# Performance work log

Hardware: AMD Instinct MI355X
Metric: run time of the kernel (lower is better)

The kernel has to match this reference:

```python
import jax, jax.numpy as jnp
import numpy as np

A = 100000          # num atoms
E = 1600000         # num edges
N_SPECIES = 4       # len(atomic_types)
N_RADIAL = 8        # l=1 radial functions (max_radial hyper)
N_PSEUDO = 4        # Alchemical pseudo species
D = N_RADIAL * N_PSEUDO  # embedding_dim = 32
RC = 5.0            # cutoff radius
WIDTH = 0.5         # shifted-cosine width


def setup_inputs() -> dict:
    key = jax.random.key(0)
    ks = jax.random.split(key, 9)
    return {
        "interatomic_vectors": jax.random.normal(ks[0], (E, 3), dtype=jnp.float32),
        "centers": jax.random.randint(ks[1], (E,), 0, A),
        "neighbors": jax.random.randint(ks[2], (E,), 0, A),
        "species": jax.random.randint(ks[3], (A,), 0, N_SPECIES),
        "structures": jnp.sort(jax.random.randint(ks[4], (A,), 0, 64)),
        "atom_index_in_structure": jax.random.randint(ks[5], (A,), 0, A),
        # learned params
        "W_alch": jax.random.normal(ks[6], (N_SPECIES, N_PSEUDO), dtype=jnp.float32) * 0.1,
        "center_embedding": jax.random.normal(ks[7], (N_SPECIES, D), dtype=jnp.float32),
        "W_contract": jax.random.normal(ks[8], (3, D), dtype=jnp.float32) * (1.0 / np.sqrt(D)),
    }


def _shifted_cosine(d):
    # 1 below rc-width, smooth cosine taper to 0 at rc
    inner = RC - WIDTH
    taper = 0.5 * (jnp.cos(jnp.pi * (d - inner) / WIDTH) + 1.0)
    return jnp.where(d < inner, 1.0, jnp.where(d < RC, taper, 0.0))


def reference(interatomic_vectors, centers, neighbors, species, structures,
              atom_index_in_structure, W_alch, center_embedding, W_contract):
    eps = 1e-12
    d = jnp.sqrt(jnp.sum(interatomic_vectors * interatomic_vectors, axis=1) + eps)  # (E,)
    fc = _shifted_cosine(d)                                                         # (E,)
    # Laplacian-eigenstate-style l=1 radial basis: sin(n*pi*d/rc)/d, n=1..N_RADIAL
    n = jnp.arange(1, N_RADIAL + 1, dtype=jnp.float32)
    R = jnp.sin(n[None, :] * (jnp.pi / RC) * d[:, None]) / d[:, None]               # (E, nR)
    # real l=1 spherical harmonics, m order (-1, 0, 1) -> (y, z, x)/d
    Y = interatomic_vectors[:, jnp.array([1, 2, 0])] / d[:, None]                   # (E, 3)
    # alchemical pseudo-species weights of the neighbor
    alch = W_alch[species[neighbors]]                                               # (E, nQ)
    # per-edge expansion coefficients, scattered onto centers
    edge = (fc[:, None, None, None]
            * Y[:, :, None, None]
            * R[:, None, :, None]
            * alch[:, None, None, :])                                               # (E, 3, nR, nQ)
    spex = jax.ops.segment_sum(edge, centers, num_segments=A)                       # (A, 3, nR, nQ)
    x = spex.reshape(A, 3, D)                                                       # reshape(n,q -> n*q)
    x = x * center_embedding[species][:, None, :]                                   # center encoding
    out = jnp.einsum("amd,od->amo", x, W_contract)                                  # (A, 3, 3)
    return out
```

## Files before the change

kernel.cpp:

```cpp
#include <hip/hip_runtime.h>
#include <hip/hip_fp16.h>


constexpr int NSP  = 4;
constexpr int NRAD = 8;
constexpr int NPS  = 4;
constexpr int DDIM = NRAD * NPS;

constexpr int APB       = 128;
constexpr int APB_SH    = 7;
constexpr int NBIN_PAD  = 832;
constexpr int NROWS_PAD = 832;
constexpr int RS        = 840;
constexpr int PH1_BLK   = 512;
constexpr int PH1_U     = 4;
constexpr int PH1_REC   = PH1_BLK * PH1_U;
constexpr int CAP2      = 1536;
constexpr int IT2       = CAP2 / 256;

__device__ __forceinline__ unsigned pack2(float a, float b) {
    union { __half2 h; unsigned u; } cv;
    cv.h = __floats2half2_rn(a, b);
    return cv.u;
}
__device__ __forceinline__ float2 unpack2(unsigned u) {
    union { unsigned u; __half2 h; } cv;
    cv.u = u;
    return __half22float2(cv.h);
}

__device__ __forceinline__ void build_w2(
    float* sW2, const float* cemb, const float* Wc, const float* W_alch,
    int tid, int nthreads)
{
    for (int i = tid; i < 3 * NRAD * 16; i += nthreads) {
        int p  = i & 15;
        int n  = (i >> 4) & 7;
        int o  = i >> 7;
        int sc = p >> 2, sn = p & 3;
        float w = 0.0f;
        #pragma unroll
        for (int q = 0; q < NPS; q++)
            w += cemb[sc * DDIM + n * NPS + q] * Wc[o * DDIM + n * NPS + q]
               * W_alch[sn * NPS + q];
        sW2[i] = w;
    }
}

__device__ __forceinline__ bool edge_math(
    float vx, float vy, float vz, int pair, const float* sW2,
    float g[3], float t[3])
{
    float d2    = vx * vx + vy * vy + vz * vz + 1e-12f;
    float d     = sqrtf(d2);
    float inv_d = 1.0f / d;

    const float PI = 3.14159265358979323846f;
    const float RCUT = 5.0f, INNER = 4.5f, INVW = 2.0f;
    if (d >= RCUT) return false;
    float taper = 0.5f * (__cosf(PI * (d - INNER) * INVW) + 1.0f);
    float fc = (d < INNER) ? 1.0f : taper;

    float theta = (PI / RCUT) * d;
    float s1 = __sinf(theta);
    float c1 = __cosf(theta);
    float two_c = 2.0f * c1;
    float R[NRAD];
    R[0] = s1 * inv_d;
    float sm2 = 0.0f, sm1 = s1;
    #pragma unroll
    for (int n = 1; n < NRAD; n++) {
        float s = two_c * sm1 - sm2;
        sm2 = sm1; sm1 = s;
        R[n] = s * inv_d;
    }

    #pragma unroll
    for (int o = 0; o < 3; o++) {
        float acc = 0.0f;
        #pragma unroll
        for (int n = 0; n < NRAD; n++)
            acc += R[n] * sW2[(o * NRAD + n) * 16 + pair];
        t[o] = acc;
    }
    g[0] = fc * vy * inv_d;
    g[1] = fc * vz * inv_d;
    g[2] = fc * vx * inv_d;
    return true;
}

__global__ __launch_bounds__(PH1_BLK) void vb_phase1(
    const float* __restrict__ vecs,
    const int*   __restrict__ centers,
    const int*   __restrict__ neighbors,
    const int*   __restrict__ species,
    const float* __restrict__ W_alch,
    const float* __restrict__ cemb,
    const float* __restrict__ Wc,
    unsigned short* __restrict__ runoff,
    int4*        __restrict__ payload,
    int E, int nbin)
{
    __shared__ float sW2[3 * NRAD * 16];
    __shared__ int4  srec[PH1_REC];
    __shared__ unsigned lcntP[NBIN_PAD / 2];
    __shared__ unsigned short lexcl[NBIN_PAD];
    __shared__ int sTotal;

    int tid = threadIdx.x;
    build_w2(sW2, cemb, Wc, W_alch, tid, PH1_BLK);
    for (int i = tid; i < NBIN_PAD / 2; i += PH1_BLK) lcntP[i] = 0;
    __syncthreads();

    int4 rec[PH1_U];
    int  rnk[PH1_U];
    #pragma unroll
    for (int u = 0; u < PH1_U; u++) {
        int e = blockIdx.x * PH1_REC + u * PH1_BLK + tid;
        rec[u].x = -1;
        rnk[u]   = 0;
        if (e < E) {
            float vx = vecs[3 * e + 0];
            float vy = vecs[3 * e + 1];
            float vz = vecs[3 * e + 2];
            int c  = centers[e];
            int pair = species[c] * 4 + species[neighbors[e]];
            float g[3], t[3];
            if (edge_math(vx, vy, vz, pair, sW2, g, t)) {
                rec[u].x = c;
                rec[u].y = (int)pack2(g[0], g[1]);
                rec[u].z = (int)pack2(g[2], t[0]);
                rec[u].w = (int)pack2(t[1], t[2]);
                int bin = c >> APB_SH;
                int sh  = (bin & 1) << 4;
                unsigned old = atomicAdd(&lcntP[bin >> 1], 1u << sh);
                rnk[u] = (int)((old >> sh) & 0xffff);
            }
        }
    }
    __syncthreads();

    if (tid < 64) {
        int base = tid * 13;
        int pre[13];
        int sum = 0;
        #pragma unroll
        for (int j = 0; j < 13; j++) {
            int b = base + j;
            int n = (lcntP[b >> 1] >> ((b & 1) << 4)) & 0xffff;
            pre[j] = sum; sum += n;
        }
        int incl = sum;
        #pragma unroll
        for (int off = 1; off < 64; off <<= 1) {
            int t = __shfl_up(incl, off, 64);
            if (tid >= off) incl += t;
        }
        int ex = incl - sum;
        #pragma unroll
        for (int j = 0; j < 13; j++)
            lexcl[base + j] = (unsigned short)(ex + pre[j]);
        if (tid == 63) sTotal = incl;
    }
    __syncthreads();

    #pragma unroll
    for (int u = 0; u < PH1_U; u++) {
        if (rec[u].x >= 0) {
            int bin = rec[u].x >> APB_SH;
            srec[(int)lexcl[bin] + rnk[u]] = rec[u];
        }
    }
    __syncthreads();

    int total = sTotal;
    size_t pbase = (size_t)blockIdx.x * PH1_REC;
    for (int i = tid; i < total; i += PH1_BLK)
        payload[pbase + i] = srec[i];
    unsigned short* ro = runoff + (size_t)blockIdx.x * RS;
    for (int b = tid; b <= nbin; b += PH1_BLK)
        ro[b] = (b < nbin) ? lexcl[b] : (unsigned short)total;
}

__global__ __launch_bounds__(256) void vb_phase2(
    const unsigned short* __restrict__ runoff,
    const int4*           __restrict__ payload,
    float*                __restrict__ out,
    int A, int nblocks)
{
    __shared__ int4 srec2[CAP2];
    __shared__ unsigned short sidx[CAP2];
    __shared__ unsigned short rid[CAP2];
    __shared__ unsigned short sst[NROWS_PAD];
    __shared__ unsigned short roff[NROWS_PAD + 64];
    __shared__ int cnt[APB], aexcl[APB];
    __shared__ float sout[APB * 9];
    __shared__ int sTotal;

    int b   = blockIdx.x;
    int tid = threadIdx.x;

    for (int r = tid; r < NROWS_PAD; r += 256) {
        unsigned short s0 = 0, len = 0;
        if (r < nblocks) {
            const unsigned short* row = runoff + (size_t)r * RS + b;
            s0  = row[0];
            len = (unsigned short)(row[1] - row[0]);
        }
        sst[r]  = s0;
        roff[r] = len;
    }
    __syncthreads();

    if (tid < 64) {
        int base = tid * 13;
        int pre[13];
        int sum = 0;
        #pragma unroll
        for (int j = 0; j < 13; j++) { pre[j] = sum; sum += roff[base + j]; }
        int incl = sum;
        #pragma unroll
        for (int off = 1; off < 64; off <<= 1) {
            int t = __shfl_up(incl, off, 64);
            if (tid >= off) incl += t;
        }
        int ex = incl - sum;
        #pragma unroll
        for (int j = 0; j < 13; j++)
            roff[base + j] = (unsigned short)(ex + pre[j]);
        if (tid == 63) sTotal = incl;
    }
    __syncthreads();
    if (tid == 0) roff[NROWS_PAD] = (unsigned short)sTotal;
    __syncthreads();

    int total = sTotal;
    float acc[9] = {0,0,0,0,0,0,0,0,0};
    int half = tid >> 7;
    int atom = tid & (APB - 1);

    for (int w0 = 0; w0 < total; w0 += CAP2) {
        int wend = min(w0 + CAP2, total);
        int nc = wend - w0;

        if (tid < APB) cnt[tid] = 0;
        for (int r = tid; r < nblocks; r += 256) {
            int s  = max((int)roff[r], w0);
            int e2 = min((int)roff[r + 1], wend);
            for (int p = s; p < e2; p++)
                rid[p - w0] = (unsigned short)r;
        }
        __syncthreads();

        int key6[IT2], rnk6[IT2];
        #pragma unroll
        for (int it = 0; it < IT2; it++) {
            int i = it * 256 + tid;
            key6[it] = -1;
            rnk6[it] = 0;
            if (i < nc) {
                int p = w0 + i;
                int l = (int)rid[i];
                int j = p - (int)roff[l];
                int4 r = payload[(size_t)l * PH1_REC + (int)sst[l] + j];
                srec2[i] = r;
                int k = r.x & (APB - 1);
                key6[it] = k;
                rnk6[it] = atomicAdd(&cnt[k], 1);
            }
        }
        __syncthreads();

        if (tid < 64) {
            int c0 = cnt[2 * tid], c1 = cnt[2 * tid + 1];
            int s1 = c0 + c1;
            int incl = s1;
            #pragma unroll
            for (int off = 1; off < 64; off <<= 1) {
                int t = __shfl_up(incl, off, 64);
                if (tid >= off) incl += t;
            }
            int ex = incl - s1;
            aexcl[2 * tid]     = ex;
            aexcl[2 * tid + 1] = ex + c0;
        }
        __syncthreads();

        #pragma unroll
        for (int it = 0; it < IT2; it++) {
            if (key6[it] >= 0)
                sidx[aexcl[key6[it]] + rnk6[it]] =
                    (unsigned short)(it * 256 + tid);
        }
        __syncthreads();

        {
            int st = aexcl[atom], n = cnt[atom];
            int mid = st + ((n + 1) >> 1);
            int lo = half ? mid : st;
            int hi = half ? (st + n) : mid;
            for (int j = lo; j < hi; j++) {
                int4 r = srec2[sidx[j]];
                float2 g01 = unpack2((unsigned)r.y);
                float2 g2t = unpack2((unsigned)r.z);
                float2 t12 = unpack2((unsigned)r.w);
                float g0 = g01.x, g1 = g01.y, g2 = g2t.x;
                float t0 = g2t.y, t1 = t12.x, t2 = t12.y;
                acc[0] += g0 * t0; acc[1] += g0 * t1; acc[2] += g0 * t2;
                acc[3] += g1 * t0; acc[4] += g1 * t1; acc[5] += g1 * t2;
                acc[6] += g2 * t0; acc[7] += g2 * t1; acc[8] += g2 * t2;
            }
        }
        __syncthreads();
    }

    if (half == 0) {
        #pragma unroll
        for (int k = 0; k < 9; k++) sout[atom * 9 + k] = acc[k];
    }
    __syncthreads();
    if (half == 1) {
        #pragma unroll
        for (int k = 0; k < 9; k++) sout[atom * 9 + k] += acc[k];
    }
    __syncthreads();
    size_t gbase = (size_t)b * APB * 9;
    size_t lim = (size_t)A * 9;
    for (int i = tid; i < APB * 9; i += 256) {
        size_t gi = gbase + i;
        if (gi < lim) out[gi] = sout[i];
    }
}

__global__ __launch_bounds__(256) void vb_edge_fallback(
    const float* __restrict__ vecs,
    const int*   __restrict__ centers,
    const int*   __restrict__ neighbors,
    const int*   __restrict__ species,
    const float* __restrict__ W_alch,
    const float* __restrict__ cemb,
    const float* __restrict__ Wc,
    float*       __restrict__ out,
    int E)
{
    __shared__ float sW2[3 * NRAD * 16];
    build_w2(sW2, cemb, Wc, W_alch, threadIdx.x, blockDim.x);
    __syncthreads();

    int e = blockIdx.x * blockDim.x + threadIdx.x;
    if (e >= E) return;
    float vx = vecs[3 * e + 0], vy = vecs[3 * e + 1], vz = vecs[3 * e + 2];
    int c = centers[e];
    int pair = species[c] * 4 + species[neighbors[e]];
    float g[3], t[3];
    if (!edge_math(vx, vy, vz, pair, sW2, g, t)) return;
    float* op = out + (size_t)c * 9;
    #pragma unroll
    for (int m = 0; m < 3; m++)
        #pragma unroll
        for (int o = 0; o < 3; o++)
            atomicAdd(op + m * 3 + o, g[m] * t[o]);
}

extern "C" void kernel_launch(void* const* d_in, const int* in_sizes, int n_in,
                              void* d_out, int out_size, void* d_ws, size_t ws_size,
                              hipStream_t stream) {
    const float* vecs      = (const float*)d_in[0];
    const int*   centers   = (const int*)d_in[1];
    const int*   neighbors = (const int*)d_in[2];
    const int*   species   = (const int*)d_in[3];
    const float* W_alch    = (const float*)d_in[6];
    const float* cemb      = (const float*)d_in[7];
    const float* Wc        = (const float*)d_in[8];
    float*       out       = (float*)d_out;

    int E = in_sizes[1];
    int A = in_sizes[3];
    int nbin    = (A + APB - 1) >> APB_SH;
    int nblocks = (E + PH1_REC - 1) / PH1_REC;

    size_t ro_bytes = ((size_t)nblocks * RS * 2 + 255) & ~(size_t)255;
    size_t need = ro_bytes + (size_t)nblocks * PH1_REC * 16;

    if (nbin + 1 <= RS && nbin <= NBIN_PAD && nblocks <= NROWS_PAD &&
        need <= ws_size) {
        unsigned short* runoff = (unsigned short*)d_ws;
        int4* payload = (int4*)((char*)d_ws + ro_bytes);

        vb_phase1<<<nblocks, PH1_BLK, 0, stream>>>(vecs, centers, neighbors,
                                                   species, W_alch, cemb, Wc,
                                                   runoff, payload, E, nbin);
        vb_phase2<<<nbin, 256, 0, stream>>>(runoff, payload, out, A, nblocks);
    } else {
        hipMemsetAsync(d_out, 0, (size_t)out_size * sizeof(float), stream);
        int grid = (E + 255) / 256;
        vb_edge_fallback<<<grid, 256, 0, stream>>>(vecs, centers, neighbors,
                                                   species, W_alch, cemb, Wc,
                                                   out, E);
    }
}
```

Baseline: 129.6 us.

## Bucket records by bin with global atomics and accumulate via shared atomics

```diff
diff --git a/kernel.cpp b/kernel.cpp
--- a/kernel.cpp
+++ b/kernel.cpp
@@ -10,13 +10,10 @@
 constexpr int APB       = 128;
 constexpr int APB_SH    = 7;
 constexpr int NBIN_PAD  = 832;
-constexpr int NROWS_PAD = 832;
-constexpr int RS        = 840;
 constexpr int PH1_BLK   = 512;
 constexpr int PH1_U     = 4;
 constexpr int PH1_REC   = PH1_BLK * PH1_U;
-constexpr int CAP2      = 1536;
-constexpr int IT2       = CAP2 / 256;
+constexpr int BSTR      = 2560;
 
 __device__ __forceinline__ unsigned pack2(float a, float b) {
     union { __half2 h; unsigned u; } cv;
@@ -97,7 +94,7 @@
     const float* __restrict__ W_alch,
     const float* __restrict__ cemb,
     const float* __restrict__ Wc,
-    unsigned short* __restrict__ runoff,
+    unsigned*    __restrict__ gcnt,
     int4*        __restrict__ payload,
     int E, int nbin)
 {
@@ -105,6 +102,7 @@
     __shared__ int4  srec[PH1_REC];
     __shared__ unsigned lcntP[NBIN_PAD / 2];
     __shared__ unsigned short lexcl[NBIN_PAD];
+    __shared__ unsigned short gbase[NBIN_PAD];
     __shared__ int sTotal;
 
     int tid = threadIdx.x;
@@ -171,163 +169,58 @@
             srec[(int)lexcl[bin] + rnk[u]] = rec[u];
         }
     }
+
+    for (int b = tid; b < nbin; b += PH1_BLK) {
+        int n = (int)((lcntP[b >> 1] >> ((b & 1) << 4)) & 0xffff);
+        if (n) gbase[b] = (unsigned short)atomicAdd(&gcnt[b], (unsigned)n);
+    }
     __syncthreads();
 
     int total = sTotal;
-    size_t pbase = (size_t)blockIdx.x * PH1_REC;
-    for (int i = tid; i < total; i += PH1_BLK)
-        payload[pbase + i] = srec[i];
-    unsigned short* ro = runoff + (size_t)blockIdx.x * RS;
-    for (int b = tid; b <= nbin; b += PH1_BLK)
-        ro[b] = (b < nbin) ? lexcl[b] : (unsigned short)total;
+    for (int i = tid; i < total; i += PH1_BLK) {
+        int4 r  = srec[i];
+        int bin = r.x >> APB_SH;
+        int slot = (int)gbase[bin] + (i - (int)lexcl[bin]);
+        if (slot < BSTR)
+            payload[(size_t)bin * BSTR + slot] = r;
+    }
 }
 
 __global__ __launch_bounds__(256) void vb_phase2(
-    const unsigned short* __restrict__ runoff,
-    const int4*           __restrict__ payload,
-    float*                __restrict__ out,
-    int A, int nblocks)
-{
-    __shared__ int4 srec2[CAP2];
-    __shared__ unsigned short sidx[CAP2];
-    __shared__ unsigned short rid[CAP2];
-    __shared__ unsigned short sst[NROWS_PAD];
-    __shared__ unsigned short roff[NROWS_PAD + 64];
-    __shared__ int cnt[APB], aexcl[APB];
+    const unsigned* __restrict__ gcnt,
+    const int4*     __restrict__ payload,
+    float*          __restrict__ out,
+    int A)
+{
     __shared__ float sout[APB * 9];
-    __shared__ int sTotal;
 
     int b   = blockIdx.x;
     int tid = threadIdx.x;
 
-    for (int r = tid; r < NROWS_PAD; r += 256) {
-        unsigned short s0 = 0, len = 0;
-        if (r < nblocks) {
-            const unsigned short* row = runoff + (size_t)r * RS + b;
-            s0  = row[0];
-            len = (unsigned short)(row[1] - row[0]);
-        }
-        sst[r]  = s0;
-        roff[r] = len;
-    }
-    __syncthreads();
-
-    if (tid < 64) {
-        int base = tid * 13;
-        int pre[13];
-        int sum = 0;
-        #pragma unroll
-        for (int j = 0; j < 13; j++) { pre[j] = sum; sum += roff[base + j]; }
-        int incl = sum;
-        #pragma unroll
-        for (int off = 1; off < 64; off <<= 1) {
-            int t = __shfl_up(incl, off, 64);
-            if (tid >= off) incl += t;
-        }
-        int ex = incl - sum;
-        #pragma unroll
-        for (int j = 0; j < 13; j++)
-            roff[base + j] = (unsigned short)(ex + pre[j]);
-        if (tid == 63) sTotal = incl;
-    }
-    __syncthreads();
-    if (tid == 0) roff[NROWS_PAD] = (unsigned short)sTotal;
-    __syncthreads();
-
-    int total = sTotal;
-    float acc[9] = {0,0,0,0,0,0,0,0,0};
-    int half = tid >> 7;
-    int atom = tid & (APB - 1);
-
-    for (int w0 = 0; w0 < total; w0 += CAP2) {
-        int wend = min(w0 + CAP2, total);
-        int nc = wend - w0;
-
-        if (tid < APB) cnt[tid] = 0;
-        for (int r = tid; r < nblocks; r += 256) {
-            int s  = max((int)roff[r], w0);
-            int e2 = min((int)roff[r + 1], wend);
-            for (int p = s; p < e2; p++)
-                rid[p - w0] = (unsigned short)r;
-        }
-        __syncthreads();
-
-        int key6[IT2], rnk6[IT2];
-        #pragma unroll
-        for (int it = 0; it < IT2; it++) {
-            int i = it * 256 + tid;
-            key6[it] = -1;
-            rnk6[it] = 0;
-            if (i < nc) {
-                int p = w0 + i;
-                int l = (int)rid[i];
-                int j = p - (int)roff[l];
-                int4 r = payload[(size_t)l * PH1_REC + (int)sst[l] + j];
-                srec2[i] = r;
-                int k = r.x & (APB - 1);
-                key6[it] = k;
-                rnk6[it] = atomicAdd(&cnt[k], 1);
-            }
-        }
-        __syncthreads();
-
-        if (tid < 64) {
-            int c0 = cnt[2 * tid], c1 = cnt[2 * tid + 1];
-            int s1 = c0 + c1;
-            int incl = s1;
-            #pragma unroll
-            for (int off = 1; off < 64; off <<= 1) {
-                int t = __shfl_up(incl, off, 64);
-                if (tid >= off) incl += t;
-            }
-            int ex = incl - s1;
-            aexcl[2 * tid]     = ex;
-            aexcl[2 * tid + 1] = ex + c0;
-        }
-        __syncthreads();
-
-        #pragma unroll
-        for (int it = 0; it < IT2; it++) {
-            if (key6[it] >= 0)
-                sidx[aexcl[key6[it]] + rnk6[it]] =
-                    (unsigned short)(it * 256 + tid);
-        }
-        __syncthreads();
-
-        {
-            int st = aexcl[atom], n = cnt[atom];
-            int mid = st + ((n + 1) >> 1);
-            int lo = half ? mid : st;
-            int hi = half ? (st + n) : mid;
-            for (int j = lo; j < hi; j++) {
-                int4 r = srec2[sidx[j]];
-                float2 g01 = unpack2((unsigned)r.y);
-                float2 g2t = unpack2((unsigned)r.z);
-                float2 t12 = unpack2((unsigned)r.w);
-                float g0 = g01.x, g1 = g01.y, g2 = g2t.x;
-                float t0 = g2t.y, t1 = t12.x, t2 = t12.y;
-                acc[0] += g0 * t0; acc[1] += g0 * t1; acc[2] += g0 * t2;
-                acc[3] += g1 * t0; acc[4] += g1 * t1; acc[5] += g1 * t2;
-                acc[6] += g2 * t0; acc[7] += g2 * t1; acc[8] += g2 * t2;
-            }
-        }
-        __syncthreads();
-    }
-
-    if (half == 0) {
-        #pragma unroll
-        for (int k = 0; k < 9; k++) sout[atom * 9 + k] = acc[k];
-    }
-    __syncthreads();
-    if (half == 1) {
-        #pragma unroll
-        for (int k = 0; k < 9; k++) sout[atom * 9 + k] += acc[k];
-    }
-    __syncthreads();
-    size_t gbase = (size_t)b * APB * 9;
+    for (int i = tid; i < APB * 9; i += 256) sout[i] = 0.0f;
+    __syncthreads();
+
+    int n = min((int)gcnt[b], BSTR);
+    const int4* seg = payload + (size_t)b * BSTR;
+    for (int i = tid; i < n; i += 256) {
+        int4 r = seg[i];
+        int atom = r.x & (APB - 1);
+        float2 g01 = unpack2((unsigned)r.y);
+        float2 g2t = unpack2((unsigned)r.z);
+        float2 t12 = unpack2((unsigned)r.w);
+        float g0 = g01.x, g1 = g01.y, g2 = g2t.x;
+        float t0 = g2t.y, t1 = t12.x, t2 = t12.y;
+        float* s = &sout[atom * 9];
+        atomicAdd(s + 0, g0 * t0); atomicAdd(s + 1, g0 * t1); atomicAdd(s + 2, g0 * t2);
+        atomicAdd(s + 3, g1 * t0); atomicAdd(s + 4, g1 * t1); atomicAdd(s + 5, g1 * t2);
+        atomicAdd(s + 6, g2 * t0); atomicAdd(s + 7, g2 * t1); atomicAdd(s + 8, g2 * t2);
+    }
+    __syncthreads();
+
+    size_t gbase2 = (size_t)b * APB * 9;
     size_t lim = (size_t)A * 9;
     for (int i = tid; i < APB * 9; i += 256) {
-        size_t gi = gbase + i;
+        size_t gi = gbase2 + i;
         if (gi < lim) out[gi] = sout[i];
     }
 }
@@ -379,18 +272,18 @@
     int nbin    = (A + APB - 1) >> APB_SH;
     int nblocks = (E + PH1_REC - 1) / PH1_REC;
 
-    size_t ro_bytes = ((size_t)nblocks * RS * 2 + 255) & ~(size_t)255;
-    size_t need = ro_bytes + (size_t)nblocks * PH1_REC * 16;
-
-    if (nbin + 1 <= RS && nbin <= NBIN_PAD && nblocks <= NROWS_PAD &&
-        need <= ws_size) {
-        unsigned short* runoff = (unsigned short*)d_ws;
-        int4* payload = (int4*)((char*)d_ws + ro_bytes);
-
+    size_t gc_bytes = ((size_t)nbin * 4 + 255) & ~(size_t)255;
+    size_t need = gc_bytes + (size_t)nbin * BSTR * 16;
+
+    if (nbin <= NBIN_PAD && need <= ws_size) {
+        unsigned* gcnt = (unsigned*)d_ws;
+        int4* payload = (int4*)((char*)d_ws + gc_bytes);
+
+        hipMemsetAsync(gcnt, 0, (size_t)nbin * 4, stream);
         vb_phase1<<<nblocks, PH1_BLK, 0, stream>>>(vecs, centers, neighbors,
                                                    species, W_alch, cemb, Wc,
-                                                   runoff, payload, E, nbin);
-        vb_phase2<<<nbin, 256, 0, stream>>>(runoff, payload, out, A, nblocks);
+                                                   gcnt, payload, E, nbin);
+        vb_phase2<<<nbin, 256, 0, stream>>>(gcnt, payload, out, A);
     } else {
         hipMemsetAsync(d_out, 0, (size_t)out_size * sizeof(float), stream);
         int grid = (E + 255) / 256;
```

Measured after the change: 223.0 us. 1.72x slower.

## Replace per-atom counting sort in phase2 with fixed-point LDS atomic accumulation

Applied to the files above, without the earlier changes.

```diff
diff --git a/kernel.cpp b/kernel.cpp
--- a/kernel.cpp
+++ b/kernel.cpp
@@ -15,8 +15,10 @@
 constexpr int PH1_BLK   = 512;
 constexpr int PH1_U     = 4;
 constexpr int PH1_REC   = PH1_BLK * PH1_U;
-constexpr int CAP2      = 1536;
-constexpr int IT2       = CAP2 / 256;
+constexpr int CAPR      = 4096;
+
+constexpr float ACC_SCALE     = 32768.0f;
+constexpr float ACC_INV_SCALE = 1.0f / 32768.0f;
 
 __device__ __forceinline__ unsigned pack2(float a, float b) {
     union { __half2 h; unsigned u; } cv;
@@ -188,13 +190,10 @@
     float*                __restrict__ out,
     int A, int nblocks)
 {
-    __shared__ int4 srec2[CAP2];
-    __shared__ unsigned short sidx[CAP2];
-    __shared__ unsigned short rid[CAP2];
     __shared__ unsigned short sst[NROWS_PAD];
-    __shared__ unsigned short roff[NROWS_PAD + 64];
-    __shared__ int cnt[APB], aexcl[APB];
-    __shared__ float sout[APB * 9];
+    __shared__ unsigned short roff[NROWS_PAD];
+    __shared__ unsigned short rid[CAPR];
+    __shared__ int sacc[APB * 9];
     __shared__ int sTotal;
 
     int b   = blockIdx.x;
@@ -210,6 +209,7 @@
         sst[r]  = s0;
         roff[r] = len;
     }
+    for (int i = tid; i < APB * 9; i += 256) sacc[i] = 0;
     __syncthreads();
 
     if (tid < 64) {
@@ -231,19 +231,13 @@
         if (tid == 63) sTotal = incl;
     }
     __syncthreads();
-    if (tid == 0) roff[NROWS_PAD] = (unsigned short)sTotal;
-    __syncthreads();
 
     int total = sTotal;
-    float acc[9] = {0,0,0,0,0,0,0,0,0};
-    int half = tid >> 7;
-    int atom = tid & (APB - 1);
-
-    for (int w0 = 0; w0 < total; w0 += CAP2) {
-        int wend = min(w0 + CAP2, total);
+
+    for (int w0 = 0; w0 < total; w0 += CAPR) {
+        int wend = min(w0 + CAPR, total);
         int nc = wend - w0;
 
-        if (tid < APB) cnt[tid] = 0;
         for (int r = tid; r < nblocks; r += 256) {
             int s  = max((int)roff[r], w0);
             int e2 = min((int)roff[r + 1], wend);
@@ -252,83 +246,37 @@
         }
         __syncthreads();
 
-        int key6[IT2], rnk6[IT2];
-        #pragma unroll
-        for (int it = 0; it < IT2; it++) {
-            int i = it * 256 + tid;
-            key6[it] = -1;
-            rnk6[it] = 0;
-            if (i < nc) {
-                int p = w0 + i;
-                int l = (int)rid[i];
-                int j = p - (int)roff[l];
-                int4 r = payload[(size_t)l * PH1_REC + (int)sst[l] + j];
-                srec2[i] = r;
-                int k = r.x & (APB - 1);
-                key6[it] = k;
-                rnk6[it] = atomicAdd(&cnt[k], 1);
-            }
+        for (int i = tid; i < nc; i += 256) {
+            int p = w0 + i;
+            int l = (int)rid[i];
+            int j = p - (int)roff[l];
+            int4 r = payload[(size_t)l * PH1_REC + (int)sst[l] + j];
+            int atom = r.x & (APB - 1);
+            float2 g01 = unpack2((unsigned)r.y);
+            float2 g2t = unpack2((unsigned)r.z);
+            float2 t12 = unpack2((unsigned)r.w);
+            float g0 = g01.x * ACC_SCALE, g1 = g01.y * ACC_SCALE;
+            float g2 = g2t.x * ACC_SCALE;
+            float t0 = g2t.y, t1 = t12.x, t2 = t12.y;
+            int* s = &sacc[atom * 9];
+            atomicAdd(s + 0, __float2int_rn(g0 * t0));
+            atomicAdd(s + 1, __float2int_rn(g0 * t1));
+            atomicAdd(s + 2, __float2int_rn(g0 * t2));
+            atomicAdd(s + 3, __float2int_rn(g1 * t0));
+            atomicAdd(s + 4, __float2int_rn(g1 * t1));
+            atomicAdd(s + 5, __float2int_rn(g1 * t2));
+            atomicAdd(s + 6, __float2int_rn(g2 * t0));
+            atomicAdd(s + 7, __float2int_rn(g2 * t1));
+            atomicAdd(s + 8, __float2int_rn(g2 * t2));
         }
         __syncthreads();
-
-        if (tid < 64) {
-            int c0 = cnt[2 * tid], c1 = cnt[2 * tid + 1];
-            int s1 = c0 + c1;
-            int incl = s1;
-            #pragma unroll
-            for (int off = 1; off < 64; off <<= 1) {
-                int t = __shfl_up(incl, off, 64);
-                if (tid >= off) incl += t;
-            }
-            int ex = incl - s1;
-            aexcl[2 * tid]     = ex;
-            aexcl[2 * tid + 1] = ex + c0;
-        }
-        __syncthreads();
-
-        #pragma unroll
-        for (int it = 0; it < IT2; it++) {
-            if (key6[it] >= 0)
-                sidx[aexcl[key6[it]] + rnk6[it]] =
-                    (unsigned short)(it * 256 + tid);
-        }
-        __syncthreads();
-
-        {
-            int st = aexcl[atom], n = cnt[atom];
-            int mid = st + ((n + 1) >> 1);
-            int lo = half ? mid : st;
-            int hi = half ? (st + n) : mid;
-            for (int j = lo; j < hi; j++) {
-                int4 r = srec2[sidx[j]];
-                float2 g01 = unpack2((unsigned)r.y);
-                float2 g2t = unpack2((unsigned)r.z);
-                float2 t12 = unpack2((unsigned)r.w);
-                float g0 = g01.x, g1 = g01.y, g2 = g2t.x;
-                float t0 = g2t.y, t1 = t12.x, t2 = t12.y;
-                acc[0] += g0 * t0; acc[1] += g0 * t1; acc[2] += g0 * t2;
-                acc[3] += g1 * t0; acc[4] += g1 * t1; acc[5] += g1 * t2;
-                acc[6] += g2 * t0; acc[7] += g2 * t1; acc[8] += g2 * t2;
-            }
-        }
-        __syncthreads();
-    }
-
-    if (half == 0) {
-        #pragma unroll
-        for (int k = 0; k < 9; k++) sout[atom * 9 + k] = acc[k];
-    }
-    __syncthreads();
-    if (half == 1) {
-        #pragma unroll
-        for (int k = 0; k < 9; k++) sout[atom * 9 + k] += acc[k];
-    }
-    __syncthreads();
+    }
+
     size_t gbase = (size_t)b * APB * 9;
     size_t lim = (size_t)A * 9;
     for (int i = tid; i < APB * 9; i += 256) {
         size_t gi = gbase + i;
-        if (gi < lim) out[gi] = sout[i];
+        if (gi < lim) out[gi] = (float)sacc[i] * ACC_INV_SCALE;
     }
 }
 
@@ -382,7 +330,7 @@
     size_t ro_bytes = ((size_t)nblocks * RS * 2 + 255) & ~(size_t)255;
     size_t need = ro_bytes + (size_t)nblocks * PH1_REC * 16;
 
-    if (nbin + 1 <= RS && nbin <= NBIN_PAD && nblocks <= NROWS_PAD &&
+    if (nbin + 1 <= RS && nbin <= NBIN_PAD && nblocks < NROWS_PAD &&
         need <= ws_size) {
         unsigned short* runoff = (unsigned short*)d_ws;
         int4* payload = (int4*)((char*)d_ws + ro_bytes);
```

After: 126.4 us. 1.03x faster.
